# Performance work log

Measured on AMD Instinct MI355X. Metric: run time of the kernel, lower is better.

## Reference

```python
import jax, jax.numpy as jnp
import numpy as np

B, N, F_IN, F_OUT, H = 4, 2048, 256, 256, 4
NEG_INF = -1e9
EDGE_PROB = 0.05
LEAKY_SLOPE = 0.2  # tf.nn.leaky_relu default alpha


def setup_inputs() -> dict:
    key = jax.random.key(0)
    k_x, k_m, k_w, k_a, k_b = jax.random.split(key, 5)
    inputs = jax.random.normal(k_x, (B, N, F_IN), dtype=jnp.float32)
    # bias: additive adjacency mask, 0 on edges / -1e9 off-edges (standard GAT)
    u = jax.random.uniform(k_m, (B, N, N), dtype=jnp.float32)
    bias = jnp.where(u < EDGE_PROB, 0.0, NEG_INF).astype(jnp.float32)
    # self-loops so every softmax row has at least one valid entry
    bias = bias.at[:, jnp.arange(N), jnp.arange(N)].set(0.0)
    # per-head learned params (uniform [0,1) init as in the original)
    W = jax.random.uniform(k_w, (H, F_IN, F_OUT), dtype=jnp.float32)
    a = jax.random.uniform(k_a, (H, F_OUT), dtype=jnp.float32)
    b = jax.random.uniform(k_b, (H, F_OUT), dtype=jnp.float32)
    return {"inputs": inputs, "bias": bias, "W": W, "a": a, "b": b}


def reference(inputs, bias, W, a, b):
    # transformed: [H, B, N, F_OUT]
    t = jnp.einsum('bnf,hfo->hbno', inputs, W) + b[:, None, None, :]
    # per-node score s = t @ a : [H, B, N]
    s = jnp.einsum('hbno,ho->hbn', t, a)
    # weights[i,j] = s[i] + s[j]  (weights + transpose)
    w = s[..., :, None] + s[..., None, :]  # [H, B, N, N]
    coefs = jax.nn.softmax(jax.nn.leaky_relu(w, negative_slope=LEAKY_SLOPE) + bias, axis=-1)
    heads = jnp.einsum('hbnm,hbmo->hbno', coefs, t)  # [H, B, N, F_OUT]
    return jnp.mean(heads, axis=0)  # (1/num_heads) * add_n(heads)
```

## Files before the change

kernel.cpp:

```cpp
#include <hip/hip_runtime.h>
#include <hip/hip_bf16.h>
#include <stdint.h>

#define H 4
#define BB 4
#define NN 2048
#define FIN 256
#define FOUT 256
#define M_TOT (BB*NN)
#define LEAKY 0.2f

typedef float f32x4 __attribute__((ext_vector_type(4)));
typedef short s16x8 __attribute__((ext_vector_type(8)));
typedef unsigned int u32;

static __device__ __forceinline__ short f2bf(float f) {
    return __builtin_bit_cast(short, __float2bfloat16(f));
}
static __device__ __forceinline__ float bf2f(short u) {
    unsigned x = ((unsigned)(unsigned short)u) << 16;
    return __builtin_bit_cast(float, x);
}
static __device__ __forceinline__ void glds16(const void* g, void* l) {
    __builtin_amdgcn_global_load_lds(
        (const __attribute__((address_space(1))) u32*)(g),
        (__attribute__((address_space(3))) u32*)(l), 16, 0, 0);
}

static __device__ __forceinline__ size_t tts_addr(int h, int b, int o, int j) {
    return ((size_t)((h * 4 + b) * 32 + (j >> 6))) * 16384
         + o * 64 + ((((j >> 3) & 7) ^ (o & 7)) << 3) + (j & 7);
}

__global__ __launch_bounds__(256) void k_wt(const float* __restrict__ W, short* __restrict__ WT) {
    __shared__ float lds[64][65];
    int bid = blockIdx.x;
    int h = bid >> 4, kt = (bid >> 2) & 3, ot = bid & 3;
    int kb = kt * 64, ob = ot * 64;
    int tx = threadIdx.x & 63, ty = threadIdx.x >> 6;
#pragma unroll
    for (int r = 0; r < 16; ++r) {
        int k_l = ty + r * 4;
        lds[tx][k_l] = W[(size_t)(h * FIN + kb + k_l) * FOUT + ob + tx];
    }
    __syncthreads();
#pragma unroll
    for (int r = 0; r < 16; ++r) {
        int o_l = ty + r * 4;
        WT[(size_t)(h * FOUT + ob + o_l) * FIN + kb + tx] = f2bf(lds[o_l][tx]);
    }
}

__global__ __launch_bounds__(256) void k_q(const float* __restrict__ W, const float* __restrict__ a,
                                           float* __restrict__ q) {
    int wv = (blockIdx.x * 256 + threadIdx.x) >> 6;
    int lane = threadIdx.x & 63;
    int h = wv >> 8, f = wv & 255;
    float4 w4 = *(const float4*)(W + (size_t)(h * FIN + f) * FOUT + lane * 4);
    float4 a4 = *(const float4*)(a + h * FOUT + lane * 4);
    float d = w4.x * a4.x + w4.y * a4.y + w4.z * a4.z + w4.w * a4.w;
#pragma unroll
    for (int off = 32; off; off >>= 1) d += __shfl_xor(d, off);
    if (lane == 0) q[h * FIN + f] = d;
}

__global__ __launch_bounds__(256) void k_c(const float* __restrict__ bvec, const float* __restrict__ a,
                                           float* __restrict__ c) {
    int h = threadIdx.x >> 6, lane = threadIdx.x & 63;
    float4 b4 = *(const float4*)(bvec + h * FOUT + lane * 4);
    float4 a4 = *(const float4*)(a + h * FOUT + lane * 4);
    float d = b4.x * a4.x + b4.y * a4.y + b4.z * a4.z + b4.w * a4.w;
#pragma unroll
    for (int off = 32; off; off >>= 1) d += __shfl_xor(d, off);
    if (lane == 0) c[h] = d;
}

__global__ __launch_bounds__(256) void k_s(const float* __restrict__ X, const float* __restrict__ q,
                                           const float* __restrict__ c, float* __restrict__ s,
                                           short* __restrict__ Xbf) {
    int m = blockIdx.x * 4 + (threadIdx.x >> 6);
    int lane = threadIdx.x & 63;
    float4 xv = *(const float4*)(X + (size_t)m * FIN + lane * 4);
    short4 xb;
    xb.x = f2bf(xv.x); xb.y = f2bf(xv.y); xb.z = f2bf(xv.z); xb.w = f2bf(xv.w);
    *(short4*)(Xbf + (size_t)m * FIN + lane * 4) = xb;
#pragma unroll
    for (int h = 0; h < H; ++h) {
        float4 qv = *(const float4*)(q + h * FIN + lane * 4);
        float d = xv.x * qv.x + xv.y * qv.y + xv.z * qv.z + xv.w * qv.w;
#pragma unroll
        for (int off = 32; off; off >>= 1) d += __shfl_xor(d, off);
        if (lane == 0) s[h * M_TOT + m] = d + c[h];
    }
}

__global__ __launch_bounds__(256) void k_mask(const float* __restrict__ bias, unsigned* __restrict__ mask) {
    size_t t = (size_t)blockIdx.x * 256 + threadIdx.x;
    const float* p = bias + t * 32;
    unsigned bits = 0;
#pragma unroll
    for (int k = 0; k < 8; ++k) {
        float4 v = *(const float4*)(p + k * 4);
        bits |= (v.x > -1.f ? 1u : 0u) << (k * 4 + 0);
        bits |= (v.y > -1.f ? 1u : 0u) << (k * 4 + 1);
        bits |= (v.z > -1.f ? 1u : 0u) << (k * 4 + 2);
        bits |= (v.w > -1.f ? 1u : 0u) << (k * 4 + 3);
    }
    mask[t] = bits;
}

__global__ __launch_bounds__(256) void k_gemm_t(const short* __restrict__ WT, const short* __restrict__ Xbf,
                                                const float* __restrict__ bvec, short* __restrict__ tTs) {
    int h = blockIdx.z;
    int ob = blockIdx.y * 64;
    int mb = blockIdx.x * 128;
    int lane = threadIdx.x & 63, w = threadIdx.x >> 6;
    int r16 = lane & 15, g = lane >> 4;
    int mw = mb + w * 32;
    f32x4 acc[4][2] = {};
    for (int k = 0; k < FIN; k += 32) {
        s16x8 afr[4], bfr[2];
#pragma unroll
        for (int fa = 0; fa < 4; ++fa)
            afr[fa] = *(const s16x8*)(WT + (size_t)(h * FOUT + ob + fa * 16 + r16) * FIN + k + g * 8);
#pragma unroll
        for (int fb = 0; fb < 2; ++fb)
            bfr[fb] = *(const s16x8*)(Xbf + (size_t)(mw + fb * 16 + r16) * FIN + k + g * 8);
#pragma unroll
        for (int fa = 0; fa < 4; ++fa)
#pragma unroll
            for (int fb = 0; fb < 2; ++fb)
                acc[fa][fb] = __builtin_amdgcn_mfma_f32_16x16x32_bf16(afr[fa], bfr[fb], acc[fa][fb], 0, 0, 0);
    }
#pragma unroll
    for (int fa = 0; fa < 4; ++fa) {
#pragma unroll
        for (int r = 0; r < 4; ++r) {
            int o = ob + fa * 16 + g * 4 + r;
            float bv = bvec[h * FOUT + o];
#pragma unroll
            for (int fb = 0; fb < 2; ++fb) {
                int m = mw + fb * 16 + r16;
                int bb = m >> 11, j = m & 2047;
                tTs[tts_addr(h, bb, o, j)] = f2bf(acc[fa][fb][r] + bv);
            }
        }
    }
}

__global__ __launch_bounds__(256, 2) void k_attn(const short* __restrict__ tTs, const float* __restrict__ s,
                                                 const unsigned* __restrict__ mask, short* __restrict__ OT) {
    __shared__ short buf[2][16384];
    __shared__ float lds_ml[2][64][4];

    int flat = blockIdx.x + 32 * (blockIdx.y + 4 * blockIdx.z);
    int swz = (flat & 7) * 64 + (flat >> 3);
    int qt = swz & 31, b = (swz >> 5) & 3, h = swz >> 7;
    int ib = qt * 64;

    int tid = threadIdx.x;
    int lane = tid & 63, w = tid >> 6;
    int r16 = lane & 15, g = lane >> 4;
    int qg = w >> 1, par = w & 1;
    int i0 = ib + qg * 32 + r16, i1 = i0 + 16;
    size_t gm = (size_t)b * NN;

    const char* slab = (const char*)(tTs + (size_t)(h * 4 + b) * 32 * 16384);
    float si0 = s[h * M_TOT + gm + i0];
    float si1 = s[h * M_TOT + gm + i1];
    const float* srow = s + h * M_TOT + gm;
    const unsigned* mk0 = mask + (gm + i0) * (NN / 32);
    const unsigned* mk1 = mask + (gm + i1) * (NN / 32);

    int rd_base = r16 * 64 + ((((par << 2) + g) ^ (r16 & 7)) << 3);

    f32x4 acc[16][2] = {};
    float m0 = -1e9f, l0 = 0.f, m1 = -1e9f, l1 = 0.f;

    {
        const char* gsrc = slab + w * 8192 + lane * 16;
#pragma unroll
        for (int k = 0; k < 8; ++k)
            glds16(gsrc + k * 1024, &buf[0][w * 4096 + k * 512]);
    }
    asm volatile("s_waitcnt vmcnt(0)" ::: "memory");
    __builtin_amdgcn_s_barrier();
    __builtin_amdgcn_sched_barrier(0);

    for (int t = 0; t < 32; ++t) {
        int cur = t & 1;
        int jw = t * 64 + par * 32;
        float4 sj0 = *(const float4*)(srow + jw + g * 8);
        float4 sj1 = *(const float4*)(srow + jw + g * 8 + 4);
        unsigned w0 = mk0[t * 2 + par] >> (g * 8);
        unsigned w1 = mk1[t * 2 + par] >> (g * 8);
        float sj[8] = {sj0.x, sj0.y, sj0.z, sj0.w, sj1.x, sj1.y, sj1.z, sj1.w};
        float sc0[8], sc1[8];
#pragma unroll
        for (int e = 0; e < 8; ++e) {
            float y0 = si0 + sj[e];
            float y1 = si1 + sj[e];
            float ly0 = fmaxf(y0, 0.2f * y0);
            float ly1 = fmaxf(y1, 0.2f * y1);
            sc0[e] = ((w0 >> e) & 1u) ? ly0 : -1e9f;
            sc1[e] = ((w1 >> e) & 1u) ? ly1 : -1e9f;
        }
        float t0 = fmaxf(fmaxf(fmaxf(sc0[0], sc0[1]), fmaxf(sc0[2], sc0[3])),
                         fmaxf(fmaxf(sc0[4], sc0[5]), fmaxf(sc0[6], sc0[7])));
        float t1 = fmaxf(fmaxf(fmaxf(sc1[0], sc1[1]), fmaxf(sc1[2], sc1[3])),
                         fmaxf(fmaxf(sc1[4], sc1[5]), fmaxf(sc1[6], sc1[7])));
        t0 = fmaxf(t0, __shfl_xor(t0, 16)); t0 = fmaxf(t0, __shfl_xor(t0, 32));
        t1 = fmaxf(t1, __shfl_xor(t1, 16)); t1 = fmaxf(t1, __shfl_xor(t1, 32));

        if (!__all((t0 <= m0 + 8.f) && (t1 <= m1 + 8.f))) {
            float mn0 = fmaxf(m0, t0), mn1 = fmaxf(m1, t1);
            float s0 = __expf(m0 - mn0), s1 = __expf(m1 - mn1);
            l0 *= s0; l1 *= s1;
#pragma unroll
            for (int f = 0; f < 16; ++f) { acc[f][0] *= s0; acc[f][1] *= s1; }
            m0 = mn0; m1 = mn1;
        }

        float ps0 = 0.f, ps1 = 0.f;
        s16x8 pb0, pb1;
#pragma unroll
        for (int e = 0; e < 8; ++e) {
            float p0 = __expf(sc0[e] - m0);
            float p1 = __expf(sc1[e] - m1);
            ps0 += p0; ps1 += p1;
            pb0[e] = f2bf(p0); pb1[e] = f2bf(p1);
        }
        ps0 += __shfl_xor(ps0, 16); ps0 += __shfl_xor(ps0, 32);
        ps1 += __shfl_xor(ps1, 16); ps1 += __shfl_xor(ps1, 32);
        l0 += ps0; l1 += ps1;

        __builtin_amdgcn_sched_barrier(0);
        if (t + 1 < 32) {
            const char* gsrc = slab + (size_t)(t + 1) * 32768 + w * 8192 + lane * 16;
#pragma unroll
            for (int k = 0; k < 8; ++k)
                glds16(gsrc + k * 1024, &buf[cur ^ 1][w * 4096 + k * 512]);
        }
        asm volatile("s_waitcnt vmcnt(8)" ::: "memory");
        __builtin_amdgcn_s_barrier();
        __builtin_amdgcn_sched_barrier(0);

        const short* bp = &buf[cur][0];
        __builtin_amdgcn_s_setprio(1);
#pragma unroll
        for (int f = 0; f < 16; ++f) {
            s16x8 af = *(const s16x8*)(bp + f * 1024 + rd_base);
            acc[f][0] = __builtin_amdgcn_mfma_f32_16x16x32_bf16(af, pb0, acc[f][0], 0, 0, 0);
            acc[f][1] = __builtin_amdgcn_mfma_f32_16x16x32_bf16(af, pb1, acc[f][1], 0, 0, 0);
        }
        __builtin_amdgcn_s_setprio(0);
        __builtin_amdgcn_sched_barrier(0);
        __builtin_amdgcn_s_barrier();
    }

    if (par) {
        lds_ml[qg][lane][0] = m0; lds_ml[qg][lane][1] = l0;
        lds_ml[qg][lane][2] = m1; lds_ml[qg][lane][3] = l1;
    }
    f32x4* ex = (f32x4*)buf;
    if (par) {
#pragma unroll
        for (int f = 0; f < 16; ++f) {
            ex[((qg * 16 + f) * 2 + 0) * 64 + lane] = acc[f][0];
            ex[((qg * 16 + f) * 2 + 1) * 64 + lane] = acc[f][1];
        }
    }
    __syncthreads();
    if (!par) {
        float mo0 = lds_ml[qg][lane][0], lo0 = lds_ml[qg][lane][1];
        float mo1 = lds_ml[qg][lane][2], lo1 = lds_ml[qg][lane][3];
        float ms0 = fmaxf(m0, mo0);
        float a0 = __expf(m0 - ms0), b0 = __expf(mo0 - ms0);
        float inv0 = 1.f / (l0 * a0 + lo0 * b0);
        float w00 = a0 * inv0, w01 = b0 * inv0;
        float ms1 = fmaxf(m1, mo1);
        float a1 = __expf(m1 - ms1), b1 = __expf(mo1 - ms1);
        float inv1 = 1.f / (l1 * a1 + lo1 * b1);
        float w10 = a1 * inv1, w11 = b1 * inv1;
        size_t ob0 = (size_t)h * FOUT * M_TOT + gm;
#pragma unroll
        for (int f = 0; f < 16; ++f) {
            f32x4 v0 = acc[f][0] * w00 + ex[((qg * 16 + f) * 2 + 0) * 64 + lane] * w01;
            f32x4 v1 = acc[f][1] * w10 + ex[((qg * 16 + f) * 2 + 1) * 64 + lane] * w11;
#pragma unroll
            for (int rr = 0; rr < 4; ++rr) {
                int o = f * 16 + g * 4 + rr;
                OT[ob0 + (size_t)o * M_TOT + i0] = f2bf(v0[rr]);
                OT[ob0 + (size_t)o * M_TOT + i1] = f2bf(v1[rr]);
            }
        }
    }
}

__global__ __launch_bounds__(256) void k_reduce(const short* __restrict__ OT, float* __restrict__ out) {
    __shared__ float lds[32][72];
    int mb = blockIdx.x * 64, obt = blockIdx.y * 32;
    int tid = threadIdx.x;
    {
        int o_l = tid >> 3;
        int m_l = (tid & 7) * 8;
        float acc[8] = {};
#pragma unroll
        for (int h = 0; h < H; ++h) {
            s16x8 v = *(const s16x8*)(OT + (size_t)(h * FOUT + obt + o_l) * M_TOT + mb + m_l);
#pragma unroll
            for (int e = 0; e < 8; ++e) acc[e] += bf2f(v[e]);
        }
#pragma unroll
        for (int e = 0; e < 8; ++e) lds[o_l][m_l + e] = acc[e] * 0.25f;
    }
    __syncthreads();
    {
        int m_l = tid >> 2;
        int o_l = (tid & 3) * 8;
        float4 v0, v1;
        v0.x = lds[o_l + 0][m_l]; v0.y = lds[o_l + 1][m_l];
        v0.z = lds[o_l + 2][m_l]; v0.w = lds[o_l + 3][m_l];
        v1.x = lds[o_l + 4][m_l]; v1.y = lds[o_l + 5][m_l];
        v1.z = lds[o_l + 6][m_l]; v1.w = lds[o_l + 7][m_l];
        float* dst = out + (size_t)(mb + m_l) * FOUT + obt + o_l;
        *(float4*)dst = v0;
        *(float4*)(dst + 4) = v1;
    }
}

extern "C" void kernel_launch(void* const* d_in, const int* in_sizes, int n_in,
                              void* d_out, int out_size, void* d_ws, size_t ws_size,
                              hipStream_t stream) {
    const float* X    = (const float*)d_in[0];
    const float* bias = (const float*)d_in[1];
    const float* W    = (const float*)d_in[2];
    const float* a    = (const float*)d_in[3];
    const float* bvec = (const float*)d_in[4];
    float* out = (float*)d_out;

    char* ws = (char*)d_ws;
    short*    Xbf  = (short*)ws;
    short*    WT   = (short*)(ws + (4u << 20));
    float*    q    = (float*)(ws + (4u << 20) + (768u << 10));
    float*    c    = q + H * FIN;
    float*    s    = (float*)(ws + (5u << 20));
    short*    tTs  = (short*)(ws + (6u << 20));
    short*    OT   = (short*)(ws + (22u << 20));
    unsigned* mask = (unsigned*)(ws + (38u << 20));

    k_wt<<<64, 256, 0, stream>>>(W, WT);
    k_q<<<256, 256, 0, stream>>>(W, a, q);
    k_c<<<1, 256, 0, stream>>>(bvec, a, c);
    k_s<<<2048, 256, 0, stream>>>(X, q, c, s, Xbf);
    k_mask<<<2048, 256, 0, stream>>>(bias, mask);
    k_gemm_t<<<dim3(64, 4, 4), 256, 0, stream>>>(WT, Xbf, bvec, tTs);
    k_attn<<<dim3(32, 4, 4), 256, 0, stream>>>(tTs, s, mask, OT);
    k_reduce<<<dim3(128, 8), 256, 0, stream>>>(OT, out);
}
```

Baseline: 139.3 us.

## Precompute exact masked row max to drop online softmax in attention

Extends the mask kernel to compute each row's maximum masked score s_j per head. Because leaky_relu is monotonic, this gives the exact softmax max up front, so the attention loop drops online rescaling, max reductions and cross-lane sum shuffles. Row sums are accumulated with an extra MFMA against a ones vector, and the exponent uses exp2 with pre-scaled inputs. The attention block grows to 512 threads covering 128 query rows, with triple-buffered dynamic LDS and one barrier per tile. The cost is extra L2 reads of s in the mask kernel and a large dynamic LDS allocation (96 KB) that may need to fit the launch limits.

```diff
diff --git a/kernel.cpp b/kernel.cpp
--- a/kernel.cpp
+++ b/kernel.cpp
@@ -8,7 +8,7 @@
 #define FIN 256
 #define FOUT 256
 #define M_TOT (BB*NN)
-#define LEAKY 0.2f
+#define LOG2E 1.44269504f
 
 typedef float f32x4 __attribute__((ext_vector_type(4)));
 typedef short s16x8 __attribute__((ext_vector_type(8)));
@@ -94,19 +94,38 @@
     }
 }
 
-__global__ __launch_bounds__(256) void k_mask(const float* __restrict__ bias, unsigned* __restrict__ mask) {
-    size_t t = (size_t)blockIdx.x * 256 + threadIdx.x;
-    const float* p = bias + t * 32;
+__global__ __launch_bounds__(256) void k_maskmax(const float* __restrict__ bias, const float* __restrict__ s,
+                                                 unsigned* __restrict__ mask, float* __restrict__ mx) {
+    int w = threadIdx.x >> 6, lane = threadIdx.x & 63;
+    int row = blockIdx.x * 4 + w;
+    const float* bp = bias + (size_t)row * NN + lane * 32;
     unsigned bits = 0;
 #pragma unroll
     for (int k = 0; k < 8; ++k) {
-        float4 v = *(const float4*)(p + k * 4);
+        float4 v = *(const float4*)(bp + k * 4);
         bits |= (v.x > -1.f ? 1u : 0u) << (k * 4 + 0);
         bits |= (v.y > -1.f ? 1u : 0u) << (k * 4 + 1);
         bits |= (v.z > -1.f ? 1u : 0u) << (k * 4 + 2);
         bits |= (v.w > -1.f ? 1u : 0u) << (k * 4 + 3);
     }
-    mask[t] = bits;
+    mask[(size_t)row * 64 + lane] = bits;
+    int b = row >> 11;
+#pragma unroll
+    for (int h = 0; h < H; ++h) {
+        const float* sp = s + h * M_TOT + b * NN + lane * 32;
+        float m = -3e38f;
+#pragma unroll
+        for (int k = 0; k < 8; ++k) {
+            float4 sv = *(const float4*)(sp + k * 4);
+            m = fmaxf(m, ((bits >> (k * 4 + 0)) & 1u) ? sv.x : -3e38f);
+            m = fmaxf(m, ((bits >> (k * 4 + 1)) & 1u) ? sv.y : -3e38f);
+            m = fmaxf(m, ((bits >> (k * 4 + 2)) & 1u) ? sv.z : -3e38f);
+            m = fmaxf(m, ((bits >> (k * 4 + 3)) & 1u) ? sv.w : -3e38f);
+        }
+#pragma unroll
+        for (int off = 32; off; off >>= 1) m = fmaxf(m, __shfl_xor(m, off));
+        if (lane == 0) mx[h * M_TOT + row] = m;
+    }
 }
 
 __global__ __launch_bounds__(256) void k_gemm_t(const short* __restrict__ WT, const short* __restrict__ Xbf,
@@ -148,15 +167,15 @@
     }
 }
 
-__global__ __launch_bounds__(256, 2) void k_attn(const short* __restrict__ tTs, const float* __restrict__ s,
-                                                 const unsigned* __restrict__ mask, short* __restrict__ OT) {
-    __shared__ short buf[2][16384];
-    __shared__ float lds_ml[2][64][4];
-
-    int flat = blockIdx.x + 32 * (blockIdx.y + 4 * blockIdx.z);
-    int swz = (flat & 7) * 64 + (flat >> 3);
-    int qt = swz & 31, b = (swz >> 5) & 3, h = swz >> 7;
-    int ib = qt * 64;
+__global__ __launch_bounds__(512, 2) void k_attn(const short* __restrict__ tTs, const float* __restrict__ s,
+                                                 const unsigned* __restrict__ mask, const float* __restrict__ mx,
+                                                 short* __restrict__ OT) {
+    extern __shared__ short smem[];
+
+    int flat = blockIdx.x + 16 * (blockIdx.y + 4 * blockIdx.z);
+    int swz = (flat & 7) * 32 + (flat >> 3);
+    int qt = swz & 15, b = (swz >> 4) & 3, h = swz >> 6;
+    int ib = qt * 128;
 
     int tid = threadIdx.x;
     int lane = tid & 63, w = tid >> 6;
@@ -166,134 +185,111 @@
     size_t gm = (size_t)b * NN;
 
     const char* slab = (const char*)(tTs + (size_t)(h * 4 + b) * 32 * 16384);
-    float si0 = s[h * M_TOT + gm + i0];
-    float si1 = s[h * M_TOT + gm + i1];
     const float* srow = s + h * M_TOT + gm;
-    const unsigned* mk0 = mask + (gm + i0) * (NN / 32);
-    const unsigned* mk1 = mask + (gm + i1) * (NN / 32);
+    float si0 = srow[i0], si1 = srow[i1];
+    float mx0 = mx[h * M_TOT + gm + i0];
+    float mx1 = mx[h * M_TOT + gm + i1];
+    float z0 = si0 + mx0, z1 = si1 + mx1;
+    float Mlog0 = fmaxf(z0, 0.2f * z0) * LOG2E;
+    float Mlog1 = fmaxf(z1, 0.2f * z1) * LOG2E;
+    float siL0 = si0 * LOG2E, siL1 = si1 * LOG2E;
+    const unsigned* mk0 = mask + (gm + i0) * 64;
+    const unsigned* mk1 = mask + (gm + i1) * 64;
 
     int rd_base = r16 * 64 + ((((par << 2) + g) ^ (r16 & 7)) << 3);
 
     f32x4 acc[16][2] = {};
-    float m0 = -1e9f, l0 = 0.f, m1 = -1e9f, l1 = 0.f;
-
-    {
-        const char* gsrc = slab + w * 8192 + lane * 16;
-#pragma unroll
-        for (int k = 0; k < 8; ++k)
-            glds16(gsrc + k * 1024, &buf[0][w * 4096 + k * 512]);
-    }
-    asm volatile("s_waitcnt vmcnt(0)" ::: "memory");
-    __builtin_amdgcn_s_barrier();
-    __builtin_amdgcn_sched_barrier(0);
+    f32x4 accl[2] = {};
+    s16x8 ones;
+#pragma unroll
+    for (int e = 0; e < 8; ++e) ones[e] = (short)0x3F80;
+
+    auto stage = [&](int tt, int slot) {
+        const char* gs = slab + (size_t)tt * 32768 + w * 1024 + (size_t)lane * 16;
+        short* ldb = smem + slot * 16384 + w * 512;
+        glds16(gs,          ldb);
+        glds16(gs +  8192,  ldb + 4096);
+        glds16(gs + 16384,  ldb + 8192);
+        glds16(gs + 24576,  ldb + 12288);
+    };
+    float4 psj0, psj1; unsigned pw0, pw1;
+    auto preload = [&](int tt) {
+        int jw = tt * 64 + par * 32;
+        psj0 = *(const float4*)(srow + jw + g * 8);
+        psj1 = *(const float4*)(srow + jw + g * 8 + 4);
+        pw0 = mk0[tt * 2 + par];
+        pw1 = mk1[tt * 2 + par];
+    };
+
+    stage(0, 0);
+    preload(0);
+    int cur = 0;
 
     for (int t = 0; t < 32; ++t) {
-        int cur = t & 1;
-        int jw = t * 64 + par * 32;
-        float4 sj0 = *(const float4*)(srow + jw + g * 8);
-        float4 sj1 = *(const float4*)(srow + jw + g * 8 + 4);
-        unsigned w0 = mk0[t * 2 + par] >> (g * 8);
-        unsigned w1 = mk1[t * 2 + par] >> (g * 8);
-        float sj[8] = {sj0.x, sj0.y, sj0.z, sj0.w, sj1.x, sj1.y, sj1.z, sj1.w};
-        float sc0[8], sc1[8];
+        int nxt = (cur == 2) ? 0 : cur + 1;
+        if (t < 31) stage(t + 1, nxt);
+
+        float sjv[8] = {psj0.x, psj0.y, psj0.z, psj0.w, psj1.x, psj1.y, psj1.z, psj1.w};
+        unsigned b0 = pw0 >> (g * 8), b1 = pw1 >> (g * 8);
+        s16x8 pb0, pb1;
 #pragma unroll
         for (int e = 0; e < 8; ++e) {
-            float y0 = si0 + sj[e];
-            float y1 = si1 + sj[e];
-            float ly0 = fmaxf(y0, 0.2f * y0);
-            float ly1 = fmaxf(y1, 0.2f * y1);
-            sc0[e] = ((w0 >> e) & 1u) ? ly0 : -1e9f;
-            sc1[e] = ((w1 >> e) & 1u) ? ly1 : -1e9f;
-        }
-        float t0 = fmaxf(fmaxf(fmaxf(sc0[0], sc0[1]), fmaxf(sc0[2], sc0[3])),
-                         fmaxf(fmaxf(sc0[4], sc0[5]), fmaxf(sc0[6], sc0[7])));
-        float t1 = fmaxf(fmaxf(fmaxf(sc1[0], sc1[1]), fmaxf(sc1[2], sc1[3])),
-                         fmaxf(fmaxf(sc1[4], sc1[5]), fmaxf(sc1[6], sc1[7])));
-        t0 = fmaxf(t0, __shfl_xor(t0, 16)); t0 = fmaxf(t0, __shfl_xor(t0, 32));
-        t1 = fmaxf(t1, __shfl_xor(t1, 16)); t1 = fmaxf(t1, __shfl_xor(t1, 32));
-
-        if (!__all((t0 <= m0 + 8.f) && (t1 <= m1 + 8.f))) {
-            float mn0 = fmaxf(m0, t0), mn1 = fmaxf(m1, t1);
-            float s0 = __expf(m0 - mn0), s1 = __expf(m1 - mn1);
-            l0 *= s0; l1 *= s1;
-#pragma unroll
-            for (int f = 0; f < 16; ++f) { acc[f][0] *= s0; acc[f][1] *= s1; }
-            m0 = mn0; m1 = mn1;
-        }
-
-        float ps0 = 0.f, ps1 = 0.f;
-        s16x8 pb0, pb1;
-#pragma unroll
-        for (int e = 0; e < 8; ++e) {
-            float p0 = __expf(sc0[e] - m0);
-            float p1 = __expf(sc1[e] - m1);
-            ps0 += p0; ps1 += p1;
-            pb0[e] = f2bf(p0); pb1[e] = f2bf(p1);
-        }
-        ps0 += __shfl_xor(ps0, 16); ps0 += __shfl_xor(ps0, 32);
-        ps1 += __shfl_xor(ps1, 16); ps1 += __shfl_xor(ps1, 32);
-        l0 += ps0; l1 += ps1;
+            float yL0 = fmaf(sjv[e], LOG2E, siL0);
+            float yL1 = fmaf(sjv[e], LOG2E, siL1);
+            float ly0 = fmaxf(yL0, 0.2f * yL0);
+            float ly1 = fmaxf(yL1, 0.2f * yL1);
+            float a0 = ((b0 >> e) & 1u) ? (ly0 - Mlog0) : -200.f;
+            float a1 = ((b1 >> e) & 1u) ? (ly1 - Mlog1) : -200.f;
+            pb0[e] = f2bf(__builtin_amdgcn_exp2f(a0));
+            pb1[e] = f2bf(__builtin_amdgcn_exp2f(a1));
+        }
 
         __builtin_amdgcn_sched_barrier(0);
-        if (t + 1 < 32) {
-            const char* gsrc = slab + (size_t)(t + 1) * 32768 + w * 8192 + lane * 16;
-#pragma unroll
-            for (int k = 0; k < 8; ++k)
-                glds16(gsrc + k * 1024, &buf[cur ^ 1][w * 4096 + k * 512]);
-        }
-        asm volatile("s_waitcnt vmcnt(8)" ::: "memory");
+        asm volatile("s_waitcnt vmcnt(4)" ::: "memory");
         __builtin_amdgcn_s_barrier();
         __builtin_amdgcn_sched_barrier(0);
 
-        const short* bp = &buf[cur][0];
+        const short* bt = smem + cur * 16384;
         __builtin_amdgcn_s_setprio(1);
 #pragma unroll
         for (int f = 0; f < 16; ++f) {
-            s16x8 af = *(const s16x8*)(bp + f * 1024 + rd_base);
+            s16x8 af = *(const s16x8*)(bt + f * 1024 + rd_base);
             acc[f][0] = __builtin_amdgcn_mfma_f32_16x16x32_bf16(af, pb0, acc[f][0], 0, 0, 0);
             acc[f][1] = __builtin_amdgcn_mfma_f32_16x16x32_bf16(af, pb1, acc[f][1], 0, 0, 0);
         }
+        accl[0] = __builtin_amdgcn_mfma_f32_16x16x32_bf16(ones, pb0, accl[0], 0, 0, 0);
+        accl[1] = __builtin_amdgcn_mfma_f32_16x16x32_bf16(ones, pb1, accl[1], 0, 0, 0);
         __builtin_amdgcn_s_setprio(0);
-        __builtin_amdgcn_sched_barrier(0);
-        __builtin_amdgcn_s_barrier();
-    }
-
-    if (par) {
-        lds_ml[qg][lane][0] = m0; lds_ml[qg][lane][1] = l0;
-        lds_ml[qg][lane][2] = m1; lds_ml[qg][lane][3] = l1;
-    }
-    f32x4* ex = (f32x4*)buf;
-    if (par) {
-#pragma unroll
-        for (int f = 0; f < 16; ++f) {
-            ex[((qg * 16 + f) * 2 + 0) * 64 + lane] = acc[f][0];
-            ex[((qg * 16 + f) * 2 + 1) * 64 + lane] = acc[f][1];
-        }
-    }
+
+        if (t < 31) preload(t + 1);
+        cur = nxt;
+    }
+
     __syncthreads();
-    if (!par) {
-        float mo0 = lds_ml[qg][lane][0], lo0 = lds_ml[qg][lane][1];
-        float mo1 = lds_ml[qg][lane][2], lo1 = lds_ml[qg][lane][3];
-        float ms0 = fmaxf(m0, mo0);
-        float a0 = __expf(m0 - ms0), b0 = __expf(mo0 - ms0);
-        float inv0 = 1.f / (l0 * a0 + lo0 * b0);
-        float w00 = a0 * inv0, w01 = b0 * inv0;
-        float ms1 = fmaxf(m1, mo1);
-        float a1 = __expf(m1 - ms1), b1 = __expf(mo1 - ms1);
-        float inv1 = 1.f / (l1 * a1 + lo1 * b1);
-        float w10 = a1 * inv1, w11 = b1 * inv1;
-        size_t ob0 = (size_t)h * FOUT * M_TOT + gm;
-#pragma unroll
-        for (int f = 0; f < 16; ++f) {
-            f32x4 v0 = acc[f][0] * w00 + ex[((qg * 16 + f) * 2 + 0) * 64 + lane] * w01;
-            f32x4 v1 = acc[f][1] * w10 + ex[((qg * 16 + f) * 2 + 1) * 64 + lane] * w11;
-#pragma unroll
-            for (int rr = 0; rr < 4; ++rr) {
-                int o = f * 16 + g * 4 + rr;
-                OT[ob0 + (size_t)o * M_TOT + i0] = f2bf(v0[rr]);
-                OT[ob0 + (size_t)o * M_TOT + i1] = f2bf(v1[rr]);
+    f32x4* ex = (f32x4*)smem;
+#pragma unroll
+    for (int qf = 0; qf < 2; ++qf) {
+        if (par) {
+#pragma unroll
+            for (int f = 0; f < 16; ++f) ex[(qg * 17 + f) * 64 + lane] = acc[f][qf];
+            ex[(qg * 17 + 16) * 64 + lane] = accl[qf];
+        }
+        __syncthreads();
+        if (!par) {
+            float lsum = accl[qf][0] + ex[(qg * 17 + 16) * 64 + lane][0];
+            float inv = 1.f / lsum;
+            int iq = qf ? i1 : i0;
+            size_t base = (size_t)h * FOUT * M_TOT + gm + iq;
+#pragma unroll
+            for (int f = 0; f < 16; ++f) {
+                f32x4 v = acc[f][qf] + ex[(qg * 17 + f) * 64 + lane];
+#pragma unroll
+                for (int rr = 0; rr < 4; ++rr) {
+                    OT[base + (size_t)(f * 16 + g * 4 + rr) * M_TOT] = f2bf(v[rr] * inv);
+                }
             }
         }
+        __syncthreads();
     }
 }
 
@@ -345,6 +341,7 @@
     float*    q    = (float*)(ws + (4u << 20) + (768u << 10));
     float*    c    = q + H * FIN;
     float*    s    = (float*)(ws + (5u << 20));
+    float*    mxp  = (float*)(ws + (5u << 20) + (256u << 10));
     short*    tTs  = (short*)(ws + (6u << 20));
     short*    OT   = (short*)(ws + (22u << 20));
     unsigned* mask = (unsigned*)(ws + (38u << 20));
@@ -353,8 +350,8 @@
     k_q<<<256, 256, 0, stream>>>(W, a, q);
     k_c<<<1, 256, 0, stream>>>(bvec, a, c);
     k_s<<<2048, 256, 0, stream>>>(X, q, c, s, Xbf);
-    k_mask<<<2048, 256, 0, stream>>>(bias, mask);
+    k_maskmax<<<2048, 256, 0, stream>>>(bias, s, mask, mxp);
     k_gemm_t<<<dim3(64, 4, 4), 256, 0, stream>>>(WT, Xbf, bvec, tTs);
-    k_attn<<<dim3(32, 4, 4), 256, 0, stream>>>(tTs, s, mask, OT);
+    k_attn<<<dim3(16, 4, 4), 512, 98304, stream>>>(tTs, s, mask, mxp, OT);
     k_reduce<<<dim3(128, 8), 256, 0, stream>>>(OT, out);
 }
```

Measured after the change: 148.9 us. +6.9%, slower.
